# Optimization experiments

Hardware: AMD Instinct MI355X
Metric: run time of the kernel (lower is better)

## Reference

```python
import jax, jax.numpy as jnp
import numpy as np

EPS = 1e-5

def _ln(x, g, b):
    m = jnp.mean(x, axis=-1, keepdims=True)
    v = jnp.mean((x - m) ** 2, axis=-1, keepdims=True)
    return (x - m) / jnp.sqrt(v + EPS) * g + b

B, SX, SY = 2, 2048, 2048
XD, YD, P, H, MULT = 1024, 1024, 64, 16, 4

def setup_inputs() -> dict:
    key = jax.random.key(0)
    ks = jax.random.split(key, 20)
    s = lambda fan: 1.0 / np.sqrt(fan)
    return {
        "x": jax.random.normal(ks[0], (B, SX, XD), jnp.float32),
        "y": jax.random.normal(ks[1], (B, SY, YD), jnp.float32),
        "gx_gamma": jnp.ones((XD,), jnp.float32),
        "gx_beta": jnp.zeros((XD,), jnp.float32),
        "gy_gamma": jnp.ones((YD,), jnp.float32),
        "gy_beta": jnp.zeros((YD,), jnp.float32),
        "Wq": jax.random.uniform(ks[2], (H, XD, P), jnp.float32, -s(XD), s(XD)),
        "bq": jax.random.uniform(ks[3], (H, P), jnp.float32, -s(XD), s(XD)),
        "Wk": jax.random.uniform(ks[4], (H, YD, P), jnp.float32, -s(YD), s(YD)),
        "bk": jax.random.uniform(ks[5], (H, P), jnp.float32, -s(YD), s(YD)),
        "Wv": jax.random.uniform(ks[6], (H, YD, P), jnp.float32, -s(YD), s(YD)),
        "bv": jax.random.uniform(ks[7], (H, P), jnp.float32, -s(YD), s(YD)),
        "Wo": jax.random.uniform(ks[8], (H * P, XD), jnp.float32, -s(H * P), s(H * P)),
        "bo": jax.random.uniform(ks[9], (XD,), jnp.float32, -s(H * P), s(H * P)),
        "gd_gamma": jnp.ones((XD,), jnp.float32),
        "gd_beta": jnp.zeros((XD,), jnp.float32),
        "W1": jax.random.uniform(ks[10], (XD, MULT * XD), jnp.float32, -s(XD), s(XD)),
        "b1": jax.random.uniform(ks[11], (MULT * XD,), jnp.float32, -s(XD), s(XD)),
        "W2": jax.random.uniform(ks[12], (MULT * XD, XD), jnp.float32, -s(MULT * XD), s(MULT * XD)),
        "b2": jax.random.uniform(ks[13], (XD,), jnp.float32, -s(MULT * XD), s(MULT * XD)),
        "mask": 1,
    }

def reference(x, y, gx_gamma, gx_beta, gy_gamma, gy_beta, Wq, bq, Wk, bk, Wv, bv,
              Wo, bo, gd_gamma, gd_beta, W1, b1, W2, b2, mask):
    xn = _ln(x, gx_gamma, gx_beta)
    yn = _ln(y, gy_gamma, gy_beta)
    # batched per-head projections: [B,S,D] x [H,D,P] -> [B,H,S,P]
    q = jnp.einsum('bsd,hdp->bhsp', xn, Wq) + bq[None, :, None, :]
    k = jnp.einsum('btd,hdp->bhtp', yn, Wk) + bk[None, :, None, :]
    v = jnp.einsum('btd,hdp->bhtp', yn, Wv) + bv[None, :, None, :]
    scores = jnp.einsum('bhsp,bhtp->bhst', q, k) * (1.0 / jnp.sqrt(jnp.float32(P)))
    attn = jax.nn.softmax(scores, axis=-1)
    if mask:
        # post-softmax strictly-upper-triangular mask (torch.triu diagonal=1)
        tri = jnp.triu(jnp.ones((SX, SY), attn.dtype), k=1)
        attn = attn * tri
    o = jnp.einsum('bhst,bhtp->bhsp', attn, v)          # [B,H,S,P]
    o = o.transpose(0, 2, 1, 3).reshape(B, SX, H * P)    # concat heads
    x2 = x + o @ Wo + bo
    h = jax.nn.gelu(_ln(x2, gd_gamma, gd_beta) @ W1 + b1, approximate=False)
    return x2 + h @ W2 + b2
```

## Files before the change

kernel.cpp:

```cpp
#include <hip/hip_runtime.h>
#include <hip/hip_bf16.h>
#include <math.h>

typedef __bf16 bf16_t;
typedef __bf16 bf16x8 __attribute__((ext_vector_type(8)));
typedef __bf16 bf16x4 __attribute__((ext_vector_type(4)));
typedef float f32x4 __attribute__((ext_vector_type(4)));

#define QSCALE 0.18033688011112042f

static __device__ __forceinline__ f32x4 mfma16(bf16x8 a, bf16x8 b, f32x4 c) {
  return __builtin_amdgcn_mfma_f32_16x16x32_bf16(a, b, c, 0, 0, 0);
}

static __device__ __forceinline__ float gelu_f(float x) {
  return 0.5f * x * (1.0f + erff(x * 0.70710678118654752440f));
}

static __device__ __forceinline__ float exp2_fast(float x) {
  float r;
  asm("v_exp_f32 %0, %1" : "=v"(r) : "v"(x));
  return r;
}

typedef __attribute__((address_space(1))) const void as1_void;
typedef __attribute__((address_space(3))) void as3_void;
static __device__ __forceinline__ void gload16(const void* g, void* s) {
  __builtin_amdgcn_global_load_lds((as1_void*)g, (as3_void*)s, 16, 0, 0);
}

static __device__ __forceinline__ long hmi(int row, int col) {
  return ((((long)(row >> 11) * 16 + (col >> 6)) * 2048) + (row & 2047)) * 64 + (col & 63);
}

__global__ __launch_bounds__(256) void prep_all(
    const float* __restrict__ Wq, const float* __restrict__ Wk, const float* __restrict__ Wv,
    const float* __restrict__ Wo, const float* __restrict__ W1, const float* __restrict__ W2,
    bf16_t* __restrict__ WqkvT, bf16_t* __restrict__ WoT, bf16_t* __restrict__ W1T,
    bf16_t* __restrict__ W2T, const float* __restrict__ x, const float* __restrict__ y,
    const float* __restrict__ gx, const float* __restrict__ bex, const float* __restrict__ gy,
    const float* __restrict__ bey, bf16_t* __restrict__ xn, bf16_t* __restrict__ yn) {
  const int bid = blockIdx.x;
  if (bid >= 3072) {
    const int lrow = bid - 3072;
    const float* in = lrow < 4096 ? x : y;
    const float* g = lrow < 4096 ? gx : gy;
    const float* be = lrow < 4096 ? bex : bey;
    bf16_t* out = lrow < 4096 ? xn : yn;
    const int row = lrow & 4095;
    const int t = threadIdx.x;
    const float4 xv = ((const float4*)(in + (long)row * 1024))[t];
    float s1 = xv.x + xv.y + xv.z + xv.w;
    float s2 = xv.x * xv.x + xv.y * xv.y + xv.z * xv.z + xv.w * xv.w;
#pragma unroll
    for (int m = 1; m < 64; m <<= 1) {
      s1 += __shfl_xor(s1, m);
      s2 += __shfl_xor(s2, m);
    }
    __shared__ float r1[4], r2[4];
    if ((t & 63) == 0) { r1[t >> 6] = s1; r2[t >> 6] = s2; }
    __syncthreads();
    s1 = r1[0] + r1[1] + r1[2] + r1[3];
    s2 = r2[0] + r2[1] + r2[2] + r2[3];
    const float mean = s1 * (1.0f / 1024.0f);
    float var = s2 * (1.0f / 1024.0f) - mean * mean;
    const float rstd = rsqrtf(fmaxf(var, 0.0f) + 1e-5f);
    const float4 gv = ((const float4*)g)[t];
    const float4 bv = ((const float4*)be)[t];
    bf16x4 o;
    o[0] = (bf16_t)((xv.x - mean) * rstd * gv.x + bv.x);
    o[1] = (bf16_t)((xv.y - mean) * rstd * gv.y + bv.y);
    o[2] = (bf16_t)((xv.z - mean) * rstd * gv.z + bv.z);
    o[3] = (bf16_t)((xv.w - mean) * rstd * gv.w + bv.w);
    *(bf16x4*)(out + (long)row * 1024 + t * 4) = o;
    return;
  }
  const float* inp;
  bf16_t* outp;
  int istride, ostride, i0, j0;
  if (bid < 768) {
    const int wsel = bid >> 8, rem = bid & 255;
    const int h = rem >> 4, xt = rem & 15;
    const float* W = wsel == 0 ? Wq : (wsel == 1 ? Wk : Wv);
    inp = W + h * 65536;
    outp = WqkvT + (long)wsel * 1048576 + h * 65536;
    istride = 64; ostride = 1024; i0 = xt * 64; j0 = 0;
  } else if (bid < 1024) {
    const int rem = bid - 768;
    inp = Wo; outp = WoT; istride = 1024; ostride = 1024;
    i0 = (rem & 15) * 64; j0 = (rem >> 4) * 64;
  } else if (bid < 2048) {
    const int rem = bid - 1024;
    inp = W1; outp = W1T; istride = 4096; ostride = 1024;
    i0 = (rem & 15) * 64; j0 = (rem >> 4) * 64;
  } else {
    const int rem = bid - 2048;
    inp = W2; outp = W2T; istride = 1024; ostride = 4096;
    i0 = (rem >> 4) * 64; j0 = (rem & 15) * 64;
  }
  __shared__ bf16_t tile[64][65];
  const int r = threadIdx.x >> 2, cs = (threadIdx.x & 3) * 16;
#pragma unroll
  for (int jj = 0; jj < 16; jj++)
    tile[cs + jj][r] = (bf16_t)inp[(long)(i0 + r) * istride + j0 + cs + jj];
  __syncthreads();
#pragma unroll
  for (int jj = 0; jj < 16; jj++)
    outp[(long)(j0 + r) * ostride + i0 + cs + jj] = tile[r][cs + jj];
}

__global__ __launch_bounds__(256) void ln_kernel(const float* __restrict__ in,
                                                 const float* __restrict__ g,
                                                 const float* __restrict__ be,
                                                 bf16_t* __restrict__ out) {
  const int row = blockIdx.x, t = threadIdx.x;
  const float4 xv = ((const float4*)(in + (long)row * 1024))[t];
  float s1 = xv.x + xv.y + xv.z + xv.w;
  float s2 = xv.x * xv.x + xv.y * xv.y + xv.z * xv.z + xv.w * xv.w;
#pragma unroll
  for (int m = 1; m < 64; m <<= 1) {
    s1 += __shfl_xor(s1, m);
    s2 += __shfl_xor(s2, m);
  }
  __shared__ float r1[4], r2[4];
  if ((t & 63) == 0) { r1[t >> 6] = s1; r2[t >> 6] = s2; }
  __syncthreads();
  s1 = r1[0] + r1[1] + r1[2] + r1[3];
  s2 = r2[0] + r2[1] + r2[2] + r2[3];
  const float mean = s1 * (1.0f / 1024.0f);
  float var = s2 * (1.0f / 1024.0f) - mean * mean;
  const float rstd = rsqrtf(fmaxf(var, 0.0f) + 1e-5f);
  const float4 gv = ((const float4*)g)[t];
  const float4 bv = ((const float4*)be)[t];
  bf16x4 o;
  o[0] = (bf16_t)((xv.x - mean) * rstd * gv.x + bv.x);
  o[1] = (bf16_t)((xv.y - mean) * rstd * gv.y + bv.y);
  o[2] = (bf16_t)((xv.z - mean) * rstd * gv.z + bv.z);
  o[3] = (bf16_t)((xv.w - mean) * rstd * gv.w + bv.w);
  *(bf16x4*)(out + (long)row * 1024 + t * 4) = o;
}

template <int EPI>
__global__ __launch_bounds__(512, 2) void gemm256(const bf16_t* __restrict__ A,
                                                  const bf16_t* __restrict__ Bt,
                                                  const float* __restrict__ bias,
                                                  void* __restrict__ Cout,
                                                  int M, int N, int K) {
  __shared__ bf16_t a_l[2][2][256 * 32];
  __shared__ bf16_t b_l[2][2][256 * 32];
  const int tid = threadIdx.x, l = tid & 63, wid = tid >> 6;
  const int wr = wid >> 2, wc = wid & 3;
  const int lr = l & 15, lg = l >> 4;
  const int orig = blockIdx.y * gridDim.x + blockIdx.x;
  const int xcd = orig & 7, ii = orig >> 3;
  const int bx = (xcd & 3) * 4 + (ii & 3);
  const int by = (xcd >> 2) * 8 + (ii >> 2);
  const int m0 = by * 256, n0 = bx * 256;
  const int sr0 = tid >> 2, sr1 = 128 + (tid >> 2);
  const int sch2 = ((tid & 3) ^ ((tid >> 3) & 3)) * 8;
  const int sl0 = sr0 * 32 + (tid & 3) * 8;
  const int sl1 = sr1 * 32 + (tid & 3) * 8;
#define STG_A(bufi, kki, kcol)                                        \
  do {                                                                \
    gload16(A + (long)(m0 + sr0) * K + (kcol) + sch2, &a_l[bufi][kki][sl0]); \
    gload16(A + (long)(m0 + sr1) * K + (kcol) + sch2, &a_l[bufi][kki][sl1]); \
  } while (0)
#define STG_B(bufi, kki, kcol)                                        \
  do {                                                                \
    gload16(Bt + (long)(n0 + sr0) * K + (kcol) + sch2, &b_l[bufi][kki][sl0]); \
    gload16(Bt + (long)(n0 + sr1) * K + (kcol) + sch2, &b_l[bufi][kki][sl1]); \
  } while (0)
  const int ch = (lg ^ ((lr >> 1) & 3)) * 8;
  const int nt = K >> 6;
  f32x4 acc[8][4] = {};
  bf16x8 af[8], bf2[2];
  STG_A(0, 0, 0); STG_B(0, 0, 0);
  STG_A(0, 1, 32); STG_B(0, 1, 32);
  STG_A(1, 0, 64); STG_B(1, 0, 64);
  asm volatile("s_waitcnt vmcnt(8)" ::: "memory");
  __builtin_amdgcn_s_barrier();
  for (int t = 0; t < nt; t++) {
    const int buf = t & 1, nbuf = buf ^ 1;
    const long kc = (long)t * 64;
#define RD_A(kki)                                                      \
  _Pragma("unroll") for (int m = 0; m < 8; m++) af[m] =                \
      *(const bf16x8*)&a_l[buf][kki][(wr * 128 + m * 16 + lr) * 32 + ch];
#define RD_B(kki, nh)                                                  \
  _Pragma("unroll") for (int j = 0; j < 2; j++) bf2[j] =               \
      *(const bf16x8*)&b_l[buf][kki][(wc * 64 + ((nh)*2 + j) * 16 + lr) * 32 + ch];
#define MM(nh)                                                         \
  __builtin_amdgcn_s_setprio(1);                                       \
  _Pragma("unroll") for (int m = 0; m < 8; m++) {                      \
    acc[m][(nh)*2 + 0] = mfma16(af[m], bf2[0], acc[m][(nh)*2 + 0]);    \
    acc[m][(nh)*2 + 1] = mfma16(af[m], bf2[1], acc[m][(nh)*2 + 1]);    \
  }                                                                    \
  __builtin_amdgcn_s_setprio(0);
    RD_A(0); RD_B(0, 0);
    if (t + 1 < nt) { STG_A(nbuf, 1, kc + 96); }
    __builtin_amdgcn_s_barrier();
    asm volatile("s_waitcnt lgkmcnt(0)" ::: "memory");
    __builtin_amdgcn_sched_barrier(0);
    MM(0);
    __builtin_amdgcn_s_barrier();
    RD_B(0, 1);
    if (t + 1 < nt) { STG_B(nbuf, 1, kc + 96); }
    if (t + 1 < nt) asm volatile("s_waitcnt vmcnt(8)" ::: "memory");
    else            asm volatile("s_waitcnt vmcnt(0)" ::: "memory");
    __builtin_amdgcn_s_barrier();
    asm volatile("s_waitcnt lgkmcnt(0)" ::: "memory");
    __builtin_amdgcn_sched_barrier(0);
    MM(1);
    __builtin_amdgcn_s_barrier();
    RD_A(1); RD_B(1, 0);
    if (t + 2 < nt) { STG_A(buf, 0, kc + 128); }
    __builtin_amdgcn_s_barrier();
    asm volatile("s_waitcnt lgkmcnt(0)" ::: "memory");
    __builtin_amdgcn_sched_barrier(0);
    MM(0);
    __builtin_amdgcn_s_barrier();
    RD_B(1, 1);
    if (t + 2 < nt) { STG_B(buf, 0, kc + 128); }
    if (t + 2 < nt)      asm volatile("s_waitcnt vmcnt(8)" ::: "memory");
    else if (t + 1 < nt) asm volatile("s_waitcnt vmcnt(4)" ::: "memory");
    __builtin_amdgcn_s_barrier();
    asm volatile("s_waitcnt lgkmcnt(0)" ::: "memory");
    __builtin_amdgcn_sched_barrier(0);
    MM(1);
    __builtin_amdgcn_s_barrier();
  }
#undef RD_A
#undef RD_B
#undef MM
#undef STG_A
#undef STG_B
#pragma unroll
  for (int m = 0; m < 8; m++)
#pragma unroll
    for (int n = 0; n < 4; n++) {
      const int row_b = m0 + wr * 128 + m * 16 + lg * 4;
      const int col = n0 + wc * 64 + n * 16 + lr;
      const float bia = bias[col];
#pragma unroll
      for (int r = 0; r < 4; r++) {
        const long idx = (long)(row_b + r) * N + col;
        if (EPI == 2) ((bf16_t*)Cout)[idx] = (bf16_t)gelu_f(acc[m][n][r] + bia);
      }
    }
}

template <int EPI, int BN, int RW>
__global__ __launch_bounds__(256) void gemm32(const bf16_t* __restrict__ A,
                                              const bf16_t* __restrict__ A2,
                                              const bf16_t* __restrict__ Bt,
                                              const float* __restrict__ bias,
                                              const float* __restrict__ biasB,
                                              const float* __restrict__ biasC,
                                              bf16_t* __restrict__ aux,
                                              void* __restrict__ Cout,
                                              int M, int N, int K) {
  constexpr int NF = BN / 32;
  constexpr int NBI = BN / 64;
  __shared__ bf16_t a_lds[3][128 * 32];
  __shared__ bf16_t b_lds[3][BN * 32];
  const int tid = threadIdx.x, l = tid & 63, w = tid >> 6;
  const int wr = w >> 1, wc = w & 1;
  const int nwg = gridDim.x * gridDim.y;
  const int orig = blockIdx.y * gridDim.x + blockIdx.x;
  const int cpx = nwg >> 3;
  const int xcd = orig & 7, ii = orig >> 3;
  const int rpr = gridDim.x / RW;
  const int bx = (xcd % rpr) * RW + (ii % RW);
  const int by = (xcd / rpr) * (cpx / RW) + (ii / RW);
  const int m0 = by * 128, n0 = bx * BN;
  const bf16_t* Ause = (EPI == 5 && n0 >= 1024) ? A2 : A;
  const int lr = l & 15, lg = l >> 4;
  long a_src[2];
  int a_dst[2];
#pragma unroll
  for (int i = 0; i < 2; i++) {
    const int row = i * 64 + (tid >> 2);
    const int sc = ((tid & 3) ^ ((row >> 1) & 3)) * 8;
    a_src[i] = (long)(m0 + row) * K + sc;
    a_dst[i] = (i * 64 + w * 16) * 32;
  }
  long b_src[NBI];
#pragma unroll
  for (int i = 0; i < NBI; i++) {
    const int row = i * 64 + (tid >> 2);
    const int sc = ((tid & 3) ^ ((row >> 1) & 3)) * 8;
    b_src[i] = (long)(n0 + row) * K + sc;
  }
  const int nk = K >> 5;
  f32x4 acc[4][NF] = {};
#pragma unroll
  for (int tt = 0; tt < 2; tt++) {
#pragma unroll
    for (int i = 0; i < 2; i++) gload16(Ause + a_src[i] + tt * 32, &a_lds[tt][a_dst[i]]);
#pragma unroll
    for (int i = 0; i < NBI; i++) gload16(Bt + b_src[i] + tt * 32, &b_lds[tt][a_dst[i]]);
  }
  int cu = 0;
  for (int t = 0; t < nk; t++) {
    if (t + 1 < nk) asm volatile("s_waitcnt vmcnt(4)" ::: "memory");
    else            asm volatile("s_waitcnt vmcnt(0)" ::: "memory");
    __builtin_amdgcn_s_barrier();
    __builtin_amdgcn_sched_barrier(0);
    if (t + 2 < nk) {
      const long k0 = (long)(t + 2) * 32;
      const int nb = cu >= 1 ? cu - 1 : 2;
#pragma unroll
      for (int i = 0; i < 2; i++) gload16(Ause + a_src[i] + k0, &a_lds[nb][a_dst[i]]);
#pragma unroll
      for (int i = 0; i < NBI; i++) gload16(Bt + b_src[i] + k0, &b_lds[nb][a_dst[i]]);
    }
    const char* ab = (const char*)&a_lds[cu][0];
    const char* bb = (const char*)&b_lds[cu][0];
    bf16x8 af[4], bfr[NF];
#pragma unroll
    for (int m = 0; m < 4; m++) {
      const int row = wr * 64 + m * 16 + lr;
      af[m] = *(const bf16x8*)(ab + row * 64 + 16 * (lg ^ ((row >> 1) & 3)));
    }
#pragma unroll
    for (int n = 0; n < NF; n++) {
      const int row = wc * (BN / 2) + n * 16 + lr;
      bfr[n] = *(const bf16x8*)(bb + row * 64 + 16 * (lg ^ ((row >> 1) & 3)));
    }
    __builtin_amdgcn_s_setprio(1);
#pragma unroll
    for (int m = 0; m < 4; m++)
#pragma unroll
      for (int n = 0; n < NF; n++) acc[m][n] = mfma16(af[m], bfr[n], acc[m][n]);
    __builtin_amdgcn_s_setprio(0);
    cu = cu < 2 ? cu + 1 : 0;
  }
#pragma unroll
  for (int m = 0; m < 4; m++)
#pragma unroll
    for (int n = 0; n < NF; n++) {
      const int row_b = m0 + wr * 64 + m * 16 + (l >> 4) * 4;
      const int col = n0 + wc * (BN / 2) + n * 16 + lr;
      if (EPI == 2) {
        const float bia = bias[col];
#pragma unroll
        for (int r = 0; r < 4; r++) {
          const long idx = (long)(row_b + r) * N + col;
          ((bf16_t*)Cout)[idx] = (bf16_t)gelu_f(acc[m][n][r] + bia);
        }
      } else if (EPI == 5) {
        if (col < 1024) {
          const float bia = bias[col];
#pragma unroll
          for (int r = 0; r < 4; r++)
            ((bf16_t*)Cout)[hmi(row_b + r, col)] = (bf16_t)((acc[m][n][r] + bia) * QSCALE);
        } else if (col < 2048) {
          const float bia = biasB[col - 1024];
#pragma unroll
          for (int r = 0; r < 4; r++)
            ((bf16_t*)Cout + 4194304)[hmi(row_b + r, col - 1024)] =
                (bf16_t)(acc[m][n][r] + bia);
        } else {
          const int vcol = col - 2048;
          const float bia = biasC[vcol];
          bf16x4 vv;
#pragma unroll
          for (int r = 0; r < 4; r++) vv[r] = (bf16_t)(acc[m][n][r] + bia);
          const int bb2 = row_b >> 11, tt = row_b & 2047;
          *(bf16x4*)&aux[(((long)(bb2 << 4) + (vcol >> 6)) * 64 + (vcol & 63)) * 2048 + tt] = vv;
        }
      }
    }
}

template <int EPI, int BN>
__global__ __launch_bounds__(256) void gemm64(const bf16_t* __restrict__ A,
                                              const bf16_t* __restrict__ Bt,
                                              const float* __restrict__ bias,
                                              const float* __restrict__ res,
                                              void* __restrict__ Cout,
                                              int M, int N, int K) {
  constexpr int NF = BN / 32;
  constexpr int NBI = BN / 32;
  __shared__ bf16_t a_lds[2][128 * 64];
  __shared__ bf16_t b_lds[2][BN * 64];
  const int tid = threadIdx.x, l = tid & 63, w = tid >> 6;
  const int wr = w >> 1, wc = w & 1;
  const int nwg = gridDim.x * gridDim.y;
  const int orig = blockIdx.y * gridDim.x + blockIdx.x;
  const int lid = (orig & 7) * (nwg >> 3) + (orig >> 3);
  const int bx = lid % gridDim.x, by = lid / gridDim.x;
  const int m0 = by * 128, n0 = bx * BN;
  const int lr = l & 15, lg = l >> 4;
  long a_src[4];
  int ldst[4];
#pragma unroll
  for (int i = 0; i < 4; i++) {
    const int row = i * 32 + w * 8 + (l >> 3);
    const int sc = ((l & 7) ^ (row & 7)) * 8;
    a_src[i] = (long)(m0 + row) * K + sc;
    ldst[i] = (i * 32 + w * 8) * 64;
  }
  long b_src[NBI];
#pragma unroll
  for (int i = 0; i < NBI; i++) {
    const int row = i * 32 + w * 8 + (l >> 3);
    const int sc = ((l & 7) ^ (row & 7)) * 8;
    b_src[i] = (long)(n0 + row) * K + sc;
  }
  const int nk = K >> 6;
  f32x4 acc[4][NF] = {};
#pragma unroll
  for (int i = 0; i < 4; i++) gload16(A + a_src[i], &a_lds[0][ldst[i]]);
#pragma unroll
  for (int i = 0; i < NBI; i++) gload16(Bt + b_src[i], &b_lds[0][ldst[i]]);
  __syncthreads();
  const int sw = (lr & 7) << 4;
  int cur = 0;
  for (int t = 0; t < nk; t++) {
    if (t + 1 < nk) {
      const long k0 = (long)(t + 1) * 64;
#pragma unroll
      for (int i = 0; i < 4; i++) gload16(A + a_src[i] + k0, &a_lds[cur ^ 1][ldst[i]]);
#pragma unroll
      for (int i = 0; i < NBI; i++) gload16(Bt + b_src[i] + k0, &b_lds[cur ^ 1][ldst[i]]);
    }
    const char* ab = (const char*)&a_lds[cur][0];
    const char* bb = (const char*)&b_lds[cur][0];
    bf16x8 af[4][2], bfr[NF][2];
#pragma unroll
    for (int m = 0; m < 4; m++) {
      const int rb = (wr * 64 + m * 16 + lr) * 128;
      af[m][0] = *(const bf16x8*)(ab + rb + ((16 * lg) ^ sw));
      af[m][1] = *(const bf16x8*)(ab + rb + ((16 * lg + 64) ^ sw));
    }
#pragma unroll
    for (int n = 0; n < NF; n++) {
      const int rb = (wc * (BN / 2) + n * 16 + lr) * 128;
      bfr[n][0] = *(const bf16x8*)(bb + rb + ((16 * lg) ^ sw));
      bfr[n][1] = *(const bf16x8*)(bb + rb + ((16 * lg + 64) ^ sw));
    }
    __builtin_amdgcn_s_setprio(1);
#pragma unroll
    for (int kk = 0; kk < 2; kk++)
#pragma unroll
      for (int m = 0; m < 4; m++)
#pragma unroll
        for (int n = 0; n < NF; n++)
          acc[m][n] = mfma16(af[m][kk], bfr[n][kk], acc[m][n]);
    __builtin_amdgcn_s_setprio(0);
    __syncthreads();
    cur ^= 1;
  }
#pragma unroll
  for (int m = 0; m < 4; m++)
#pragma unroll
    for (int n = 0; n < NF; n++) {
      const int row_b = m0 + wr * 64 + m * 16 + (l >> 4) * 4;
      const int col = n0 + wc * (BN / 2) + n * 16 + lr;
      const float bia = bias[col];
#pragma unroll
      for (int r = 0; r < 4; r++) {
        const long idx = (long)(row_b + r) * N + col;
        ((float*)Cout)[idx] = acc[m][n][r] + bia + res[idx];
      }
    }
}

__global__ __launch_bounds__(256) void attn_kernel(const bf16_t* __restrict__ qhm,
                                                   const bf16_t* __restrict__ khm,
                                                   const bf16_t* __restrict__ vtg,
                                                   bf16_t* __restrict__ og,
                                                   const int* __restrict__ maskp) {
  const int T = 2048, HP = 1024;
  __shared__ bf16_t k_lds[2][64 * 64];
  __shared__ bf16_t vt_lds[2][64 * 64];
  __shared__ bf16_t p_lds[4 * 32 * 72];
  const int bh = blockIdx.x, b = bh >> 4, h = bh & 15;
  const int q0 = blockIdx.y * 128;
  const int tid = threadIdx.x, l = tid & 63, w = tid >> 6;
  const int lr = l & 15, lg = l >> 4, lg4 = lg * 4;
  const int srow0 = q0 + w * 32 + lr;
  const bf16_t* kbase = khm + (long)bh * T * 64;
  const bf16_t* vbase = vtg + (long)bh * 64 * T;
  bf16x8 qf[2][2];
#pragma unroll
  for (int g = 0; g < 2; g++) {
    const bf16_t* qr = qhm + ((long)bh * 2048 + srow0 + g * 16) * 64 + lg * 8;
    qf[g][0] = *(const bf16x8*)qr;
    qf[g][1] = *(const bf16x8*)(qr + 32);
  }
  bf16_t* pl = &p_lds[w * 32 * 72];
  float lpart[2] = {0.0f, 0.0f};
  f32x4 oat[4][2] = {};

  const int swz = (lr & 7) << 4;
  const int fo0 = lr * 128 + ((16 * lg) ^ swz);
  const int fo1 = lr * 128 + ((64 + 16 * lg) ^ swz);

  const bool do_mask = (maskp[0] != 0);
  const int nM = do_mask ? (q0 >> 6) : 0;
  const int nt = T >> 6;

  const int sch = l & 7, srow8 = l >> 3;
  int cur = 0;
  {
    const bool needV = (nM == 0);
#pragma unroll
    for (int i = 0; i < 2; i++) {
      const int row = (i * 4 + w) * 8 + srow8;
      const int sc = (sch ^ (row & 7)) * 8;
      gload16(kbase + (long)row * 64 + sc, &k_lds[0][(i * 4 + w) * 512]);
      if (needV) gload16(vbase + (long)row * 2048 + 0 + sc, &vt_lds[0][(i * 4 + w) * 512]);
    }
  }
  __syncthreads();

  for (int t = 0; t < nt; t++) {
    const int t0 = t << 6;
    const int mode = (t < nM) ? 0 : ((do_mask && t < nM + 2) ? 1 : 2);
    if (t + 1 < nt) {
      const int t1 = (t + 1) << 6;
      const bool needV = (t + 1) >= nM;
#pragma unroll
      for (int i = 0; i < 2; i++) {
        const int row = (i * 4 + w) * 8 + srow8;
        const int sc = (sch ^ (row & 7)) * 8;
        gload16(kbase + (long)(t1 + row) * 64 + sc, &k_lds[cur ^ 1][(i * 4 + w) * 512]);
        if (needV)
          gload16(vbase + (long)row * 2048 + t1 + sc, &vt_lds[cur ^ 1][(i * 4 + w) * 512]);
      }
    }
    const char* kb = (const char*)&k_lds[cur][0];
    f32x4 sacc[4][2];
    __builtin_amdgcn_s_setprio(1);
#pragma unroll
    for (int n = 0; n < 4; n++) {
      bf16x8 kf0 = *(const bf16x8*)(kb + n * 2048 + fo0);
      bf16x8 kf1 = *(const bf16x8*)(kb + n * 2048 + fo1);
#pragma unroll
      for (int g = 0; g < 2; g++) {
        f32x4 z = {0.0f, 0.0f, 0.0f, 0.0f};
        z = mfma16(kf0, qf[g][0], z);
        sacc[n][g] = mfma16(kf1, qf[g][1], z);
      }
    }
    __builtin_amdgcn_s_setprio(0);
    float pv[2][4][4];
#pragma unroll
    for (int g = 0; g < 2; g++) {
      float psn[4];
#pragma unroll
      for (int n = 0; n < 4; n++) {
        pv[g][n][0] = exp2_fast(sacc[n][g][0]);
        pv[g][n][1] = exp2_fast(sacc[n][g][1]);
        pv[g][n][2] = exp2_fast(sacc[n][g][2]);
        pv[g][n][3] = exp2_fast(sacc[n][g][3]);
        psn[n] = (pv[g][n][0] + pv[g][n][1]) + (pv[g][n][2] + pv[g][n][3]);
      }
      lpart[g] += (psn[0] + psn[1]) + (psn[2] + psn[3]);
    }
    if (mode > 0) {
#pragma unroll
      for (int g = 0; g < 2; g++)
#pragma unroll
        for (int n = 0; n < 4; n++) {
          bf16x4 pk;
#pragma unroll
          for (int r = 0; r < 4; r++) {
            float v = pv[g][n][r];
            if (mode == 1 && (t0 + n * 16 + lg4 + r) <= srow0 + g * 16) v = 0.0f;
            pk[r] = (bf16_t)v;
          }
          *(bf16x4*)&pl[(g * 16 + lr) * 72 + n * 16 + lg4] = pk;
        }
      const char* vtb = (const char*)&vt_lds[cur][0];
      __builtin_amdgcn_s_setprio(1);
#pragma unroll
      for (int kk = 0; kk < 2; kk++) {
        bf16x8 pb0 = *(bf16x8*)&pl[lr * 72 + kk * 32 + lg * 8];
        bf16x8 pb1 = *(bf16x8*)&pl[(16 + lr) * 72 + kk * 32 + lg * 8];
        const int fkk = lr * 128 + ((kk * 64 + 16 * lg) ^ swz);
#pragma unroll
        for (int np = 0; np < 4; np++) {
          bf16x8 vtf = *(const bf16x8*)(vtb + np * 2048 + fkk);
          oat[np][0] = mfma16(vtf, pb0, oat[np][0]);
          oat[np][1] = mfma16(vtf, pb1, oat[np][1]);
        }
      }
      __builtin_amdgcn_s_setprio(0);
    }
    __syncthreads();
    cur ^= 1;
  }
  float inv[2];
#pragma unroll
  for (int g = 0; g < 2; g++) {
    float lsum = lpart[g];
    lsum += __shfl_xor(lsum, 16);
    lsum += __shfl_xor(lsum, 32);
    inv[g] = 1.0f / lsum;
  }
#pragma unroll
  for (int g = 0; g < 2; g++)
#pragma unroll
    for (int np = 0; np < 4; np++) {
      bf16x4 o4;
#pragma unroll
      for (int r = 0; r < 4; r++) o4[r] = (bf16_t)(oat[np][g][r] * inv[g]);
      *(bf16x4*)&pl[(g * 16 + lr) * 72 + np * 16 + lg4] = o4;
    }
  const int es = l >> 2, ec = (l & 3) * 16;
#pragma unroll
  for (int g = 0; g < 2; g++) {
    bf16x8 o0 = *(bf16x8*)&pl[(g * 16 + es) * 72 + ec];
    bf16x8 o1 = *(bf16x8*)&pl[(g * 16 + es) * 72 + ec + 8];
    bf16_t* orow = og + (long)(b * 2048 + q0 + w * 32 + g * 16 + es) * HP + h * 64 + ec;
    *(bf16x8*)&orow[0] = o0;
    *(bf16x8*)&orow[8] = o1;
  }
}

extern "C" void kernel_launch(void* const* d_in, const int* in_sizes, int n_in,
                              void* d_out, int out_size, void* d_ws, size_t ws_size,
                              hipStream_t stream) {
  const float* x = (const float*)d_in[0];
  const float* y = (const float*)d_in[1];
  const float* gxg = (const float*)d_in[2];
  const float* gxb = (const float*)d_in[3];
  const float* gyg = (const float*)d_in[4];
  const float* gyb = (const float*)d_in[5];
  const float* Wq = (const float*)d_in[6];
  const float* bq = (const float*)d_in[7];
  const float* Wk = (const float*)d_in[8];
  const float* bk = (const float*)d_in[9];
  const float* Wv = (const float*)d_in[10];
  const float* bv = (const float*)d_in[11];
  const float* Wo = (const float*)d_in[12];
  const float* bo = (const float*)d_in[13];
  const float* gdg = (const float*)d_in[14];
  const float* gdb = (const float*)d_in[15];
  const float* W1 = (const float*)d_in[16];
  const float* b1 = (const float*)d_in[17];
  const float* W2 = (const float*)d_in[18];
  const float* b2 = (const float*)d_in[19];
  const int* maskp = (const int*)d_in[20];
  float* out = (float*)d_out;

  char* ws = (char*)d_ws;
  const long MB = 1024 * 1024;
  bf16_t* xn = (bf16_t*)(ws + 0);
  bf16_t* yn = (bf16_t*)(ws + 8 * MB);
  bf16_t* WqkvT = (bf16_t*)(ws + 16 * MB);
  bf16_t* WoT = (bf16_t*)(ws + 22 * MB);
  bf16_t* W1T = (bf16_t*)(ws + 24 * MB);
  bf16_t* W2T = (bf16_t*)(ws + 32 * MB);
  bf16_t* qhm = (bf16_t*)(ws + 40 * MB);
  bf16_t* vTb = (bf16_t*)(ws + 64 * MB);
  bf16_t* ob = (bf16_t*)(ws + 0);
  bf16_t* xd = (bf16_t*)(ws + 8 * MB);
  bf16_t* hb = (bf16_t*)(ws + 40 * MB);
  bf16_t* khm = qhm + 4194304;

  prep_all<<<11264, 256, 0, stream>>>(Wq, Wk, Wv, Wo, W1, W2, WqkvT, WoT, W1T, W2T, x, y, gxg,
                                      gxb, gyg, gyb, xn, yn);
  gemm32<5, 128, 12><<<dim3(24, 32), 256, 0, stream>>>(xn, yn, WqkvT, bq, bk, bv, vTb, qhm,
                                                       4096, 3072, 1024);
  attn_kernel<<<dim3(32, 16), 256, 0, stream>>>(qhm, khm, vTb, ob, maskp);
  gemm64<1, 64><<<dim3(16, 32), 256, 0, stream>>>(ob, WoT, bo, x, out, 4096, 1024, 1024);
  ln_kernel<<<4096, 256, 0, stream>>>(out, gdg, gdb, xd);
  gemm256<2><<<dim3(16, 16), 512, 0, stream>>>(xd, W1T, b1, hb, 4096, 4096, 1024);
  gemm64<1, 64><<<dim3(16, 32), 256, 0, stream>>>(hb, W2T, b2, out, out, 4096, 1024, 4096);
}
```

Measured before the change: 239.3 us.

## Use 256x256 GEMM for QKV projection and split-K atomic GEMM for W2

Generalizes the 256x256 tile GEMM with an XCD-aware remap parameter, an alternate A input and extra bias pointers. The fused QKV projection moves onto it from the 128-row gemm32, and gemm32 is deleted. The final W2 GEMM (K=4096) now uses a 4-way split-K launch that accumulates into the residual output with float atomics, which gives it more workgroups. The goal is larger tiles with more operand reuse and better CU occupancy on the long-K GEMM, at the cost of atomic traffic and nondeterministic summation order.

```diff
diff --git a/kernel.cpp b/kernel.cpp
--- a/kernel.cpp
+++ b/kernel.cpp
@@ -140,10 +140,14 @@
   *(bf16x4*)(out + (long)row * 1024 + t * 4) = o;
 }
 
-template <int EPI>
+template <int EPI, int RW>
 __global__ __launch_bounds__(512, 2) void gemm256(const bf16_t* __restrict__ A,
+                                                  const bf16_t* __restrict__ A2,
                                                   const bf16_t* __restrict__ Bt,
                                                   const float* __restrict__ bias,
+                                                  const float* __restrict__ biasB,
+                                                  const float* __restrict__ biasC,
+                                                  bf16_t* __restrict__ aux,
                                                   void* __restrict__ Cout,
                                                   int M, int N, int K) {
   __shared__ bf16_t a_l[2][2][256 * 32];
@@ -151,37 +155,50 @@
   const int tid = threadIdx.x, l = tid & 63, wid = tid >> 6;
   const int wr = wid >> 2, wc = wid & 3;
   const int lr = l & 15, lg = l >> 4;
-  const int orig = blockIdx.y * gridDim.x + blockIdx.x;
-  const int xcd = orig & 7, ii = orig >> 3;
-  const int bx = (xcd & 3) * 4 + (ii & 3);
-  const int by = (xcd >> 2) * 8 + (ii >> 2);
+  const int nwg = gridDim.x * gridDim.y * gridDim.z;
+  const int orig = (blockIdx.z * gridDim.y + blockIdx.y) * gridDim.x + blockIdx.x;
+  int bx, by, ks = 0;
+  if (EPI == 6) {
+    const int lid = (orig & 7) * (nwg >> 3) + (orig >> 3);
+    bx = lid % gridDim.x;
+    by = (lid / gridDim.x) % gridDim.y;
+    ks = lid / (gridDim.x * gridDim.y);
+  } else {
+    const int cpx = nwg >> 3;
+    const int xcd = orig & 7, ii = orig >> 3;
+    const int rpr = gridDim.x / RW;
+    bx = (xcd % rpr) * RW + (ii % RW);
+    by = (xcd / rpr) * (cpx / RW) + (ii / RW);
+  }
   const int m0 = by * 256, n0 = bx * 256;
+  const long kbase = (EPI == 6) ? (long)ks << 10 : 0;
+  const int nt = (EPI == 6) ? 16 : (K >> 6);
+  const bf16_t* Ause = (EPI == 5 && n0 >= 1024) ? A2 : A;
   const int sr0 = tid >> 2, sr1 = 128 + (tid >> 2);
   const int sch2 = ((tid & 3) ^ ((tid >> 3) & 3)) * 8;
   const int sl0 = sr0 * 32 + (tid & 3) * 8;
   const int sl1 = sr1 * 32 + (tid & 3) * 8;
-#define STG_A(bufi, kki, kcol)                                        \
-  do {                                                                \
-    gload16(A + (long)(m0 + sr0) * K + (kcol) + sch2, &a_l[bufi][kki][sl0]); \
-    gload16(A + (long)(m0 + sr1) * K + (kcol) + sch2, &a_l[bufi][kki][sl1]); \
+#define STG_A(bufi, kki, kcol)                                                     \
+  do {                                                                             \
+    gload16(Ause + (long)(m0 + sr0) * K + (kcol) + sch2, &a_l[bufi][kki][sl0]);    \
+    gload16(Ause + (long)(m0 + sr1) * K + (kcol) + sch2, &a_l[bufi][kki][sl1]);    \
   } while (0)
-#define STG_B(bufi, kki, kcol)                                        \
-  do {                                                                \
-    gload16(Bt + (long)(n0 + sr0) * K + (kcol) + sch2, &b_l[bufi][kki][sl0]); \
-    gload16(Bt + (long)(n0 + sr1) * K + (kcol) + sch2, &b_l[bufi][kki][sl1]); \
+#define STG_B(bufi, kki, kcol)                                                     \
+  do {                                                                             \
+    gload16(Bt + (long)(n0 + sr0) * K + (kcol) + sch2, &b_l[bufi][kki][sl0]);      \
+    gload16(Bt + (long)(n0 + sr1) * K + (kcol) + sch2, &b_l[bufi][kki][sl1]);      \
   } while (0)
   const int ch = (lg ^ ((lr >> 1) & 3)) * 8;
-  const int nt = K >> 6;
   f32x4 acc[8][4] = {};
   bf16x8 af[8], bf2[2];
-  STG_A(0, 0, 0); STG_B(0, 0, 0);
-  STG_A(0, 1, 32); STG_B(0, 1, 32);
-  STG_A(1, 0, 64); STG_B(1, 0, 64);
+  STG_A(0, 0, kbase + 0); STG_B(0, 0, kbase + 0);
+  STG_A(0, 1, kbase + 32); STG_B(0, 1, kbase + 32);
+  STG_A(1, 0, kbase + 64); STG_B(1, 0, kbase + 64);
   asm volatile("s_waitcnt vmcnt(8)" ::: "memory");
   __builtin_amdgcn_s_barrier();
   for (int t = 0; t < nt; t++) {
     const int buf = t & 1, nbuf = buf ^ 1;
-    const long kc = (long)t * 64;
+    const long kc = kbase + (long)t * 64;
 #define RD_A(kki)                                                      \
   _Pragma("unroll") for (int m = 0; m < 8; m++) af[m] =                \
       *(const bf16x8*)&a_l[buf][kki][(wr * 128 + m * 16 + lr) * 32 + ch];
@@ -239,113 +256,19 @@
     for (int n = 0; n < 4; n++) {
       const int row_b = m0 + wr * 128 + m * 16 + lg * 4;
       const int col = n0 + wc * 64 + n * 16 + lr;
-      const float bia = bias[col];
-#pragma unroll
-      for (int r = 0; r < 4; r++) {
-        const long idx = (long)(row_b + r) * N + col;
-        if (EPI == 2) ((bf16_t*)Cout)[idx] = (bf16_t)gelu_f(acc[m][n][r] + bia);
-      }
-    }
-}
-
-template <int EPI, int BN, int RW>
-__global__ __launch_bounds__(256) void gemm32(const bf16_t* __restrict__ A,
-                                              const bf16_t* __restrict__ A2,
-                                              const bf16_t* __restrict__ Bt,
-                                              const float* __restrict__ bias,
-                                              const float* __restrict__ biasB,
-                                              const float* __restrict__ biasC,
-                                              bf16_t* __restrict__ aux,
-                                              void* __restrict__ Cout,
-                                              int M, int N, int K) {
-  constexpr int NF = BN / 32;
-  constexpr int NBI = BN / 64;
-  __shared__ bf16_t a_lds[3][128 * 32];
-  __shared__ bf16_t b_lds[3][BN * 32];
-  const int tid = threadIdx.x, l = tid & 63, w = tid >> 6;
-  const int wr = w >> 1, wc = w & 1;
-  const int nwg = gridDim.x * gridDim.y;
-  const int orig = blockIdx.y * gridDim.x + blockIdx.x;
-  const int cpx = nwg >> 3;
-  const int xcd = orig & 7, ii = orig >> 3;
-  const int rpr = gridDim.x / RW;
-  const int bx = (xcd % rpr) * RW + (ii % RW);
-  const int by = (xcd / rpr) * (cpx / RW) + (ii / RW);
-  const int m0 = by * 128, n0 = bx * BN;
-  const bf16_t* Ause = (EPI == 5 && n0 >= 1024) ? A2 : A;
-  const int lr = l & 15, lg = l >> 4;
-  long a_src[2];
-  int a_dst[2];
-#pragma unroll
-  for (int i = 0; i < 2; i++) {
-    const int row = i * 64 + (tid >> 2);
-    const int sc = ((tid & 3) ^ ((row >> 1) & 3)) * 8;
-    a_src[i] = (long)(m0 + row) * K + sc;
-    a_dst[i] = (i * 64 + w * 16) * 32;
-  }
-  long b_src[NBI];
-#pragma unroll
-  for (int i = 0; i < NBI; i++) {
-    const int row = i * 64 + (tid >> 2);
-    const int sc = ((tid & 3) ^ ((row >> 1) & 3)) * 8;
-    b_src[i] = (long)(n0 + row) * K + sc;
-  }
-  const int nk = K >> 5;
-  f32x4 acc[4][NF] = {};
-#pragma unroll
-  for (int tt = 0; tt < 2; tt++) {
-#pragma unroll
-    for (int i = 0; i < 2; i++) gload16(Ause + a_src[i] + tt * 32, &a_lds[tt][a_dst[i]]);
-#pragma unroll
-    for (int i = 0; i < NBI; i++) gload16(Bt + b_src[i] + tt * 32, &b_lds[tt][a_dst[i]]);
-  }
-  int cu = 0;
-  for (int t = 0; t < nk; t++) {
-    if (t + 1 < nk) asm volatile("s_waitcnt vmcnt(4)" ::: "memory");
-    else            asm volatile("s_waitcnt vmcnt(0)" ::: "memory");
-    __builtin_amdgcn_s_barrier();
-    __builtin_amdgcn_sched_barrier(0);
-    if (t + 2 < nk) {
-      const long k0 = (long)(t + 2) * 32;
-      const int nb = cu >= 1 ? cu - 1 : 2;
-#pragma unroll
-      for (int i = 0; i < 2; i++) gload16(Ause + a_src[i] + k0, &a_lds[nb][a_dst[i]]);
-#pragma unroll
-      for (int i = 0; i < NBI; i++) gload16(Bt + b_src[i] + k0, &b_lds[nb][a_dst[i]]);
-    }
-    const char* ab = (const char*)&a_lds[cu][0];
-    const char* bb = (const char*)&b_lds[cu][0];
-    bf16x8 af[4], bfr[NF];
-#pragma unroll
-    for (int m = 0; m < 4; m++) {
-      const int row = wr * 64 + m * 16 + lr;
-      af[m] = *(const bf16x8*)(ab + row * 64 + 16 * (lg ^ ((row >> 1) & 3)));
-    }
-#pragma unroll
-    for (int n = 0; n < NF; n++) {
-      const int row = wc * (BN / 2) + n * 16 + lr;
-      bfr[n] = *(const bf16x8*)(bb + row * 64 + 16 * (lg ^ ((row >> 1) & 3)));
-    }
-    __builtin_amdgcn_s_setprio(1);
-#pragma unroll
-    for (int m = 0; m < 4; m++)
-#pragma unroll
-      for (int n = 0; n < NF; n++) acc[m][n] = mfma16(af[m], bfr[n], acc[m][n]);
-    __builtin_amdgcn_s_setprio(0);
-    cu = cu < 2 ? cu + 1 : 0;
-  }
-#pragma unroll
-  for (int m = 0; m < 4; m++)
-#pragma unroll
-    for (int n = 0; n < NF; n++) {
-      const int row_b = m0 + wr * 64 + m * 16 + (l >> 4) * 4;
-      const int col = n0 + wc * (BN / 2) + n * 16 + lr;
       if (EPI == 2) {
         const float bia = bias[col];
 #pragma unroll
         for (int r = 0; r < 4; r++) {
           const long idx = (long)(row_b + r) * N + col;
           ((bf16_t*)Cout)[idx] = (bf16_t)gelu_f(acc[m][n][r] + bia);
+        }
+      } else if (EPI == 6) {
+        const float bia = (ks == 0) ? bias[col] : 0.0f;
+#pragma unroll
+        for (int r = 0; r < 4; r++) {
+          const long idx = (long)(row_b + r) * N + col;
+          atomicAdd(&((float*)Cout)[idx], acc[m][n][r] + bia);
         }
       } else if (EPI == 5) {
         if (col < 1024) {
@@ -663,11 +586,13 @@
 
   prep_all<<<11264, 256, 0, stream>>>(Wq, Wk, Wv, Wo, W1, W2, WqkvT, WoT, W1T, W2T, x, y, gxg,
                                       gxb, gyg, gyb, xn, yn);
-  gemm32<5, 128, 12><<<dim3(24, 32), 256, 0, stream>>>(xn, yn, WqkvT, bq, bk, bv, vTb, qhm,
-                                                       4096, 3072, 1024);
+  gemm256<5, 3><<<dim3(12, 16), 512, 0, stream>>>(xn, yn, WqkvT, bq, bk, bv, vTb, qhm, 4096,
+                                                  3072, 1024);
   attn_kernel<<<dim3(32, 16), 256, 0, stream>>>(qhm, khm, vTb, ob, maskp);
   gemm64<1, 64><<<dim3(16, 32), 256, 0, stream>>>(ob, WoT, bo, x, out, 4096, 1024, 1024);
   ln_kernel<<<4096, 256, 0, stream>>>(out, gdg, gdb, xd);
-  gemm256<2><<<dim3(16, 16), 512, 0, stream>>>(xd, W1T, b1, hb, 4096, 4096, 1024);
-  gemm64<1, 64><<<dim3(16, 32), 256, 0, stream>>>(hb, W2T, b2, out, out, 4096, 1024, 4096);
-}
+  gemm256<2, 4><<<dim3(16, 16), 512, 0, stream>>>(xd, nullptr, W1T, b1, nullptr, nullptr,
+                                                  nullptr, hb, 4096, 4096, 1024);
+  gemm256<6, 4><<<dim3(4, 16, 4), 512, 0, stream>>>(hb, nullptr, W2T, b2, nullptr, nullptr,
+                                                    nullptr, out, 4096, 1024, 4096);
+}
```

Result: slower. 268.2 us (+12.1%).
